# Kernel optimization log

Measured on AMD Instinct MI355X. Metric: run time of the kernel, lower is better.

Reference implementation:

```python
import jax, jax.numpy as jnp
import numpy as np

WIDTH = 1024

def setup_inputs() -> dict:
    key = jax.random.key(0)
    ks = jax.random.split(key, 5)
    x = jax.random.normal(ks[0], (4, 4096, WIDTH), dtype=jnp.float32)
    # LayerNorm params
    ln_gamma = jnp.ones((WIDTH,), dtype=jnp.float32)
    ln_beta = jnp.zeros((WIDTH,), dtype=jnp.float32)
    # Linear params (torch nn.Linear init: U(-1/sqrt(fan_in), 1/sqrt(fan_in)))
    bound = 1.0 / np.sqrt(WIDTH)
    w1 = jax.random.uniform(ks[1], (WIDTH, WIDTH), jnp.float32, -bound, bound)
    b1 = jax.random.uniform(ks[2], (WIDTH,), jnp.float32, -bound, bound)
    w2 = jax.random.uniform(ks[3], (WIDTH, WIDTH), jnp.float32, -bound, bound)
    b2 = jax.random.uniform(ks[4], (WIDTH,), jnp.float32, -bound, bound)
    return {"x": x, "ln_gamma": ln_gamma, "ln_beta": ln_beta,
            "w1": w1, "b1": b1, "w2": w2, "b2": b2}

def _layernorm(x, gamma, beta, eps=1e-5):
    mu = jnp.mean(x, axis=-1, keepdims=True)
    var = jnp.mean(jnp.square(x - mu), axis=-1, keepdims=True)
    return (x - mu) * jax.lax.rsqrt(var + eps) * gamma + beta

def reference(x, ln_gamma, ln_beta, w1, b1, w2, b2):
    # Pre-norm residual MLP: x + W2 @ gelu(W1 @ LN(x) + b1) + b2
    h = _layernorm(x, ln_gamma, ln_beta)
    h = jnp.einsum('bsd,ed->bse', h, w1) + b1  # w stored as [out, in] like torch
    h = jax.nn.gelu(h, approximate=False)      # torch nn.GELU default = exact erf
    # dropout p=0.0 -> identity
    h = jnp.einsum('bsd,ed->bse', h, w2) + b2
    return x + h
```

## Files before the change

### kernel.cpp

```cpp
#include <hip/hip_runtime.h>
#include <hip/hip_bf16.h>
#include <math.h>

typedef __bf16 bf16x8 __attribute__((ext_vector_type(8)));
typedef float f32x4 __attribute__((ext_vector_type(4)));

#define GAS __attribute__((address_space(1)))
#define LAS __attribute__((address_space(3)))

static __device__ __forceinline__ void load16(const void* g, void* l) {
    __builtin_amdgcn_global_load_lds((const GAS void*)g, (LAS void*)l, 16, 0, 0);
}

struct __align__(8) bh4 { __hip_bfloat16 x, y, z, w; };

__global__ __launch_bounds__(256) void pre_kernel(
        const float* __restrict__ x, const float* __restrict__ gamma,
        const float* __restrict__ beta, const float* __restrict__ w1,
        const float* __restrict__ w2, __hip_bfloat16* __restrict__ hn,
        __hip_bfloat16* __restrict__ w1b, __hip_bfloat16* __restrict__ w2b, int nln) {
    if ((int)blockIdx.x >= nln) {
        const int i = (blockIdx.x - nln) * 256 + threadIdx.x;
        float4 a = ((const float4*)w1)[i];
        float4 b = ((const float4*)w2)[i];
        bh4 r1, r2;
        r1.x = __float2bfloat16(a.x); r1.y = __float2bfloat16(a.y);
        r1.z = __float2bfloat16(a.z); r1.w = __float2bfloat16(a.w);
        r2.x = __float2bfloat16(b.x); r2.y = __float2bfloat16(b.y);
        r2.z = __float2bfloat16(b.z); r2.w = __float2bfloat16(b.w);
        ((bh4*)w1b)[i] = r1;
        ((bh4*)w2b)[i] = r2;
        return;
    }
    const int row  = (blockIdx.x << 2) + (threadIdx.x >> 6);
    const int lane = threadIdx.x & 63;
    const float4* px = (const float4*)(x + (size_t)row * 1024);
    float4 v[4];
    float s = 0.f;
#pragma unroll
    for (int i = 0; i < 4; ++i) {
        v[i] = px[lane + (i << 6)];
        s += v[i].x + v[i].y + v[i].z + v[i].w;
    }
#pragma unroll
    for (int o = 32; o; o >>= 1) s += __shfl_xor(s, o, 64);
    const float mu = s * (1.0f / 1024.0f);
    float vs = 0.f;
#pragma unroll
    for (int i = 0; i < 4; ++i) {
        float a = v[i].x - mu, b = v[i].y - mu, c = v[i].z - mu, d = v[i].w - mu;
        vs += a * a + b * b + c * c + d * d;
    }
#pragma unroll
    for (int o = 32; o; o >>= 1) vs += __shfl_xor(vs, o, 64);
    const float rs = rsqrtf(vs * (1.0f / 1024.0f) + 1e-5f);
    const float4* pg = (const float4*)gamma;
    const float4* pb = (const float4*)beta;
    bh4* po = (bh4*)(hn + (size_t)row * 1024);
#pragma unroll
    for (int i = 0; i < 4; ++i) {
        const int idx = lane + (i << 6);
        float4 g = pg[idx], bb = pb[idx];
        bh4 r;
        r.x = __float2bfloat16((v[i].x - mu) * rs * g.x + bb.x);
        r.y = __float2bfloat16((v[i].y - mu) * rs * g.y + bb.y);
        r.z = __float2bfloat16((v[i].z - mu) * rs * g.z + bb.z);
        r.w = __float2bfloat16((v[i].w - mu) * rs * g.w + bb.w);
        po[idx] = r;
    }
}

template <int EPI>
__global__ __launch_bounds__(256) void gemm_kernel(
        const __hip_bfloat16* __restrict__ A,
        const __hip_bfloat16* __restrict__ B,
        const float* __restrict__ bias,
        const float* __restrict__ resid,
        __hip_bfloat16* __restrict__ outb,
        float* __restrict__ outf) {
    constexpr int K = 1024, N = 1024;
    __shared__ __align__(16) char sA[16384];
    __shared__ __align__(16) char sB[16384];

    const int tid  = threadIdx.x;
    const int lane = tid & 63;
    const int w    = tid >> 6;
    const int wm   = (w >> 1) * 64;
    const int wn   = (w & 1) * 64;
    const int bm   = blockIdx.x * 128;
    const int bn   = blockIdx.y * 128;

    const int f = lane & 15;
    const int h = lane >> 4;

    const int srow = tid >> 3;
    const int lA_chunk = (tid & 7) ^ (srow & 7);
    const int lB_chunk = (tid & 7) ^ ((tid >> 5) & 7);
    const __hip_bfloat16* sa = A + (size_t)(bm + srow) * K + lA_chunk * 8;
    const __hip_bfloat16* sb = B + (size_t)(bn + srow) * K + lB_chunk * 8;
    char* dA = sA + tid * 16;
    char* dB = sB + tid * 16;

    const int pxk = (f & 7) * 16;
    const int px0 = (h * 16) ^ pxk;
    const int px1 = ((4 + h) * 16) ^ pxk;
    const char* aBase = sA + (wm + f) * 128;
    const char* bBase = sB + (wn + 4 * f) * 128;

    f32x4 acc[4][4] = {};

    for (int kt = 0; kt < K; kt += 64) {
#pragma unroll
        for (int q = 0; q < 4; ++q) {
            load16(sa + kt + q * 32 * K, dA + q * 4096);
            load16(sb + kt + q * 32 * K, dB + q * 4096);
        }
        __syncthreads();
#pragma unroll
        for (int c = 0; c < 2; ++c) {
            const int px = c ? px1 : px0;
            bf16x8 af[4], bf[4];
#pragma unroll
            for (int i = 0; i < 4; ++i)
                af[i] = *(const bf16x8*)(aBase + i * 2048 + px);
#pragma unroll
            for (int j = 0; j < 4; ++j)
                bf[j] = *(const bf16x8*)(bBase + j * 128 + px);
#pragma unroll
            for (int i = 0; i < 4; ++i)
#pragma unroll
                for (int j = 0; j < 4; ++j)
                    acc[i][j] = __builtin_amdgcn_mfma_f32_16x16x32_bf16(af[i], bf[j], acc[i][j], 0, 0, 0);
        }
        __syncthreads();
    }

    const int colb = bn + wn + f * 4;
    const float4 bias4 = *(const float4*)(bias + colb);
#pragma unroll
    for (int i = 0; i < 4; ++i) {
#pragma unroll
        for (int r = 0; r < 4; ++r) {
            const size_t grow = (size_t)(bm + wm + i * 16 + h * 4 + r);
            float v0 = acc[i][0][r] + bias4.x;
            float v1 = acc[i][1][r] + bias4.y;
            float v2 = acc[i][2][r] + bias4.z;
            float v3 = acc[i][3][r] + bias4.w;
            if (EPI == 0) {
                bh4 o;
                o.x = __float2bfloat16(0.5f * v0 * (1.0f + erff(v0 * 0.70710678118654752f)));
                o.y = __float2bfloat16(0.5f * v1 * (1.0f + erff(v1 * 0.70710678118654752f)));
                o.z = __float2bfloat16(0.5f * v2 * (1.0f + erff(v2 * 0.70710678118654752f)));
                o.w = __float2bfloat16(0.5f * v3 * (1.0f + erff(v3 * 0.70710678118654752f)));
                *(bh4*)(outb + grow * N + colb) = o;
            } else {
                const float4 rs = *(const float4*)(resid + grow * N + colb);
                float4 o = {v0 + rs.x, v1 + rs.y, v2 + rs.z, v3 + rs.w};
                *(float4*)(outf + grow * N + colb) = o;
            }
        }
    }
}

extern "C" void kernel_launch(void* const* d_in, const int* in_sizes, int n_in,
                              void* d_out, int out_size, void* d_ws, size_t ws_size,
                              hipStream_t stream) {
    const float* x     = (const float*)d_in[0];
    const float* gamma = (const float*)d_in[1];
    const float* beta  = (const float*)d_in[2];
    const float* w1    = (const float*)d_in[3];
    const float* b1    = (const float*)d_in[4];
    const float* w2    = (const float*)d_in[5];
    const float* b2    = (const float*)d_in[6];
    float* out = (float*)d_out;

    const int M = in_sizes[0] / 1024;

    char* ws = (char*)d_ws;
    __hip_bfloat16* hn  = (__hip_bfloat16*)ws;
    __hip_bfloat16* h1  = (__hip_bfloat16*)(ws + (size_t)M * 2048);
    __hip_bfloat16* w1b = (__hip_bfloat16*)(ws + (size_t)M * 4096);
    __hip_bfloat16* w2b = (__hip_bfloat16*)(ws + (size_t)M * 4096 + 2097152);

    const int nln = M / 4;
    pre_kernel<<<nln + 1024, 256, 0, stream>>>(x, gamma, beta, w1, w2, hn, w1b, w2b, nln);
    gemm_kernel<0><<<dim3(M / 128, 8), 256, 0, stream>>>(hn, w1b, b1, nullptr, h1, nullptr);
    gemm_kernel<1><<<dim3(M / 128, 8), 256, 0, stream>>>(h1, w2b, b2, x, nullptr, out);
}
```

Measured before the change: 227.3 us.

## Double-buffer GEMM LDS tiles with K=32 steps and prefetch next tile

Result: no change. 229.4 us (+1.0%).

```diff
diff --git a/kernel.cpp b/kernel.cpp
--- a/kernel.cpp
+++ b/kernel.cpp
@@ -79,8 +79,7 @@
         __hip_bfloat16* __restrict__ outb,
         float* __restrict__ outf) {
     constexpr int K = 1024, N = 1024;
-    __shared__ __align__(16) char sA[16384];
-    __shared__ __align__(16) char sB[16384];
+    __shared__ __align__(16) char lds[32768];
 
     const int tid  = threadIdx.x;
     const int lane = tid & 63;
@@ -89,50 +88,58 @@
     const int wn   = (w & 1) * 64;
     const int bm   = blockIdx.x * 128;
     const int bn   = blockIdx.y * 128;
-
     const int f = lane & 15;
     const int h = lane >> 4;
 
-    const int srow = tid >> 3;
-    const int lA_chunk = (tid & 7) ^ (srow & 7);
-    const int lB_chunk = (tid & 7) ^ ((tid >> 5) & 7);
-    const __hip_bfloat16* sa = A + (size_t)(bm + srow) * K + lA_chunk * 8;
-    const __hip_bfloat16* sb = B + (size_t)(bn + srow) * K + lB_chunk * 8;
-    char* dA = sA + tid * 16;
-    char* dB = sB + tid * 16;
+    const __hip_bfloat16* gA0 = A + (size_t)(bm + (tid >> 2)) * K + (tid & 3) * 8;
+    const __hip_bfloat16* gA1 = gA0 + (size_t)64 * K;
+    const int u  = (tid & 7) ^ ((tid >> 3) & 7);
+    const int rr = 2 * (tid >> 3) + (u >> 2);
+    const __hip_bfloat16* gB0 = B + (size_t)(bn + rr) * K + (u & 3) * 8;
+    const __hip_bfloat16* gB1 = gB0 + (size_t)64 * K;
+    char* dA = lds + tid * 16;
+    char* dB = lds + 16384 + tid * 16;
 
-    const int pxk = (f & 7) * 16;
-    const int px0 = (h * 16) ^ pxk;
-    const int px1 = ((4 + h) * 16) ^ pxk;
-    const char* aBase = sA + (wm + f) * 128;
-    const char* bBase = sB + (wn + 4 * f) * 128;
+    const char* aAddr = lds + (wm + f) * 64 + h * 16;
+    const char* bAddr[4];
+#pragma unroll
+    for (int j = 0; j < 4; ++j) {
+        const int pr0 = 2 * f + (j >> 1);
+        const int c3  = ((((j & 1) << 2) | h) ^ (pr0 & 7));
+        bAddr[j] = lds + 16384 + wn * 64 + pr0 * 128 + c3 * 16;
+    }
 
     f32x4 acc[4][4] = {};
 
-    for (int kt = 0; kt < K; kt += 64) {
+    load16(gA0, dA);
+    load16(gA1, dA + 4096);
+    load16(gB0, dB);
+    load16(gB1, dB + 4096);
+
 #pragma unroll
-        for (int q = 0; q < 4; ++q) {
-            load16(sa + kt + q * 32 * K, dA + q * 4096);
-            load16(sb + kt + q * 32 * K, dB + q * 4096);
+    for (int kt = 0; kt < 32; ++kt) {
+        __syncthreads();
+        const int cur = (kt & 1) * 8192;
+        if (kt + 1 < 32) {
+            const int nxt = ((kt + 1) & 1) * 8192;
+            const int go  = (kt + 1) * 32;
+            load16(gA0 + go, dA + nxt);
+            load16(gA1 + go, dA + nxt + 4096);
+            load16(gB0 + go, dB + nxt);
+            load16(gB1 + go, dB + nxt + 4096);
         }
-        __syncthreads();
+        bf16x8 af[4], bf[4];
 #pragma unroll
-        for (int c = 0; c < 2; ++c) {
-            const int px = c ? px1 : px0;
-            bf16x8 af[4], bf[4];
+        for (int i = 0; i < 4; ++i)
+            af[i] = *(const bf16x8*)(aAddr + cur + i * 1024);
 #pragma unroll
-            for (int i = 0; i < 4; ++i)
-                af[i] = *(const bf16x8*)(aBase + i * 2048 + px);
+        for (int j = 0; j < 4; ++j)
+            bf[j] = *(const bf16x8*)(bAddr[j] + cur);
+#pragma unroll
+        for (int i = 0; i < 4; ++i)
 #pragma unroll
             for (int j = 0; j < 4; ++j)
-                bf[j] = *(const bf16x8*)(bBase + j * 128 + px);
-#pragma unroll
-            for (int i = 0; i < 4; ++i)
-#pragma unroll
-                for (int j = 0; j < 4; ++j)
-                    acc[i][j] = __builtin_amdgcn_mfma_f32_16x16x32_bf16(af[i], bf[j], acc[i][j], 0, 0, 0);
-        }
-        __syncthreads();
+                acc[i][j] = __builtin_amdgcn_mfma_f32_16x16x32_bf16(af[i], bf[j], acc[i][j], 0, 0, 0);
     }
 
     const int colb = bn + wn + f * 4;
```
